# Optimization experiments

Measured on AMD Instinct MI355X. Metric: run time of the kernel, lower is better.

## Reference

```python
import jax, jax.numpy as jnp
import numpy as np

B, C, P, NG, NCLS, HID, N, IMG = 2, 256, 7, 2, 81, 1024, 512, 800
STRIDES = [4, 8, 16, 32]
SCALE = 56.0  # roi_map_level_scale


def _roi_align(feat, rois, pooled, scale, ng):
    """torchvision-legacy (aligned=False) ROI Align. feat [B,C,H,W], rois [N,5]."""
    Bf, Cf, H, W = feat.shape
    ft = jnp.transpose(feat, (0, 2, 3, 1))  # [B,H,W,C]
    b = rois[:, 0].astype(jnp.int32)
    x1, y1, x2, y2 = (rois[:, i] * scale for i in (1, 2, 3, 4))
    rw = jnp.maximum(x2 - x1, 1.0)
    rh = jnp.maximum(y2 - y1, 1.0)
    # sample grid per output bin: ng points per axis, centered in sub-bins
    g = (jnp.arange(pooled)[:, None] + (jnp.arange(ng)[None, :] + 0.5) / ng).reshape(-1)  # [P*ng]
    ys = y1[:, None] + g[None, :] * (rh / pooled)[:, None]  # [N,S]
    xs = x1[:, None] + g[None, :] * (rw / pooled)[:, None]

    def axis(coord, size):
        valid = (coord >= -1.0) & (coord <= size)
        c = jnp.clip(coord, 0.0, size - 1)
        lo = jnp.floor(c).astype(jnp.int32)
        hi = jnp.minimum(lo + 1, size - 1)
        return valid, lo, hi, c - lo

    vy, ylo, yhi, fy = axis(ys, H)
    vx, xlo, xhi, fx = axis(xs, W)
    bb = b[:, None, None]

    def gather(yi, xi):
        return ft[bb, yi[:, :, None], xi[:, None, :], :]  # [N,S,S,C]

    wy = fy[:, :, None, None]
    wx = fx[:, None, :, None]
    val = ((1 - wy) * (1 - wx) * gather(ylo, xlo) + (1 - wy) * wx * gather(ylo, xhi)
           + wy * (1 - wx) * gather(yhi, xlo) + wy * wx * gather(yhi, xhi))
    val = jnp.where((vy[:, :, None] & vx[:, None, :])[..., None], val, 0.0)
    val = val.reshape(-1, pooled, ng, pooled, ng, Cf).mean(axis=(2, 4))  # [N,P,P,C]
    return jnp.transpose(val, (0, 3, 1, 2))  # [N,C,P,P]


def setup_inputs() -> dict:
    key = jax.random.key(0)
    ks = jax.random.split(key, 16)
    feats = {}
    for i, s in enumerate(STRIDES):
        hw = IMG // s
        feats[f"p{i+2}"] = jax.random.normal(ks[i], (B, C, hw, hw), jnp.float32)
    # realistic proposals: batch idx + boxes with sizes 16..512 px
    bidx = jax.random.randint(ks[4], (N,), 0, B).astype(jnp.float32)
    sw = 2.0 ** jax.random.uniform(ks[5], (N,), minval=4.0, maxval=9.0)
    sh = 2.0 ** jax.random.uniform(ks[6], (N,), minval=4.0, maxval=9.0)
    x1 = jax.random.uniform(ks[7], (N,)) * (IMG - sw)
    y1 = jax.random.uniform(ks[8], (N,)) * (IMG - sh)
    rois = jnp.stack([bidx, x1, y1, x1 + sw - 1, y1 + sh - 1], axis=1)
    D = C * P * P
    inp = dict(feats, rois=rois,
               w1=0.01 * jax.random.normal(ks[9], (HID, D), jnp.float32),
               b1=jnp.zeros((HID,), jnp.float32),
               w2=0.01 * jax.random.normal(ks[10], (HID, HID), jnp.float32),
               b2=jnp.zeros((HID,), jnp.float32),
               w_cls=0.01 * jax.random.normal(ks[11], (NCLS, HID), jnp.float32),
               b_cls=jnp.zeros((NCLS,), jnp.float32),
               w_reg=0.001 * jax.random.normal(ks[12], (NCLS * 4, HID), jnp.float32),
               b_reg=jnp.zeros((NCLS * 4,), jnp.float32))
    return inp


def reference(p2, p3, p4, p5, rois, w1, b1, w2, b2, w_cls, b_cls, w_reg, b_reg):
    feats = [p2, p3, p4, p5]
    # FPN level assignment (same math as torch: log2(sqrt(hw)/scale + 1e-6), floor, clamp)
    rh = rois[:, 4] - rois[:, 2] + 1
    rw = rois[:, 3] - rois[:, 1] + 1
    levels = jnp.clip(jnp.floor(jnp.log2(jnp.sqrt(rh * rw) / SCALE + 1e-6)), 0, 3).astype(jnp.int32)
    # dispatch: compute each ROI on its assigned level (masked combine == gather/sort-scatter)
    pooled = jnp.zeros((rois.shape[0], C, P, P), rois.dtype)
    for l, feat in enumerate(feats):
        pl = _roi_align(feat, rois, P, 1.0 / STRIDES[l], NG)
        pooled = pooled + jnp.where((levels == l)[:, None, None, None], pl, 0.0)
    x = pooled.reshape(pooled.shape[0], -1)  # [N, C*P*P]
    x = jax.nn.relu(x @ w1.T + b1)
    x = jax.nn.relu(x @ w2.T + b2)
    x_cls = x @ w_cls.T + b_cls
    x_reg = x @ w_reg.T + b_reg  # TEST mode, not class-agnostic: no gather
    cls_probs = jax.nn.softmax(x_cls, axis=1)
    rois_out = rois.reshape(B, -1, 5)
    cls_probs = cls_probs.reshape(B, rois_out.shape[1], -1)
    bbox_preds = x_reg.reshape(B, rois_out.shape[1], -1)
    return rois_out, cls_probs, bbox_preds
```

## Files before the change

kernel.cpp:

```cpp
#include <hip/hip_runtime.h>
#include <hip/hip_bf16.h>
#include <math.h>

#define NROI   512
#define CCH    256
#define POOLP  7
#define DDIM   12544
#define HIDN   1024
#define NCLS   81
#define NREG   324
#define NHEAD  512
#define OUT_ROIS   2560
#define OUT_CLS    (512*81)

typedef __attribute__((ext_vector_type(4))) float f32x4;
typedef __attribute__((ext_vector_type(8))) short bf16x8;

static __device__ __forceinline__ unsigned short f2bf(float x) {
    __hip_bfloat16 h = __float2bfloat16(x);
    return *reinterpret_cast<unsigned short*>(&h);
}
static __device__ __forceinline__ float bf2f(unsigned short u) {
    unsigned int b = ((unsigned int)u) << 16;
    return *reinterpret_cast<float*>(&b);
}

__global__ void copy_rois_k(const float* __restrict__ rois, float* __restrict__ out) {
    int i = blockIdx.x * 256 + threadIdx.x;
    if (i < OUT_ROIS) out[i] = rois[i];
}

__global__ __launch_bounds__(256) void cvt_bf16_k(const float4* __restrict__ in,
                                                  ushort4* __restrict__ out, int n4) {
    int i = blockIdx.x * 256 + threadIdx.x;
    if (i >= n4) return;
    float4 v = in[i];
    ushort4 o;
    o.x = f2bf(v.x); o.y = f2bf(v.y); o.z = f2bf(v.z); o.w = f2bf(v.w);
    out[i] = o;
}

__global__ __launch_bounds__(256) void pack_head_k(const float* __restrict__ wc,
                                                   const float* __restrict__ wr,
                                                   unsigned short* __restrict__ Wh) {
    int i = blockIdx.x * 256 + threadIdx.x;
    int r = i >> 10, c = i & 1023;
    float v = (r < NCLS) ? wc[r * HIDN + c]
            : (r < NCLS + NREG) ? wr[(r - NCLS) * HIDN + c] : 0.f;
    Wh[i] = f2bf(v);
}

__global__ __launch_bounds__(256) void permute_w1_k(const float* __restrict__ w1,
                                                    unsigned short* __restrict__ w1b) {
    __shared__ unsigned short lw[49 * 258];
    int n = blockIdx.x, t = threadIdx.x;
    const float* src = w1 + (size_t)n * DDIM;
#pragma unroll
    for (int k = t; k < DDIM; k += 256) {
        int c = k / 49;
        int s = k - c * 49;
        lw[s * 258 + c] = f2bf(src[k]);
    }
    __syncthreads();
    unsigned int* dst = (unsigned int*)(w1b + (size_t)n * DDIM);
    for (int j2 = t; j2 < DDIM / 2; j2 += 256) {
        int s  = j2 >> 7;
        int c2 = (j2 & 127) << 1;
        unsigned int v = lw[s * 258 + c2] | ((unsigned int)lw[s * 258 + c2 + 1] << 16);
        dst[j2] = v;
    }
}

__global__ __launch_bounds__(256) void transpose_cvt_k(const float* __restrict__ in,
                                                       unsigned short* __restrict__ out,
                                                       int S) {
    __shared__ float tile[32][33];
    int b  = blockIdx.z;
    int s0 = blockIdx.x * 32, c0 = blockIdx.y * 32;
    int s  = s0 + threadIdx.x;
#pragma unroll
    for (int j = 0; j < 32; j += 8) {
        int c = c0 + threadIdx.y + j;
        tile[threadIdx.y + j][threadIdx.x] = (s < S) ? in[((size_t)b * CCH + c) * S + s] : 0.f;
    }
    __syncthreads();
    int c = c0 + threadIdx.x;
#pragma unroll
    for (int j = 0; j < 32; j += 8) {
        int s2 = s0 + threadIdx.y + j;
        if (s2 < S) out[((size_t)b * S + s2) * CCH + c] = f2bf(tile[threadIdx.x][threadIdx.y + j]);
    }
}

__global__ __launch_bounds__(256) void roi_align_k(const unsigned short* __restrict__ f0,
                                                   const unsigned short* __restrict__ f1,
                                                   const unsigned short* __restrict__ f2,
                                                   const unsigned short* __restrict__ f3,
                                                   const float* __restrict__ rois,
                                                   unsigned short* __restrict__ xpool) {
    __shared__ float s_f[16];
    __shared__ int   s_lo[16], s_hi[16], s_v[16];

    int py = blockIdx.x, r = blockIdx.y, t = threadIdx.x;

    float r0  = rois[r * 5 + 0];
    float rx1 = rois[r * 5 + 1], ry1 = rois[r * 5 + 2];
    float rx2 = rois[r * 5 + 3], ry2 = rois[r * 5 + 4];
    int b = (int)r0;

    float aw = rx2 - rx1 + 1.f, ah = ry2 - ry1 + 1.f;
    float lvf = floorf(log2f(sqrtf(ah * aw) / 56.f + 1e-6f));
    int lv = (int)fminf(fmaxf(lvf, 0.f), 3.f);

    const unsigned short* F = (lv == 0) ? f0 : (lv == 1) ? f1 : (lv == 2) ? f2 : f3;
    int HW      = (lv == 0) ? 200 : (lv == 1) ? 100 : (lv == 2) ? 50 : 25;
    float scale = (lv == 0) ? 0.25f : (lv == 1) ? 0.125f : (lv == 2) ? 0.0625f : 0.03125f;

    float x1 = rx1 * scale, yy1 = ry1 * scale;
    float x2 = rx2 * scale, yy2 = ry2 * scale;
    float rw = fmaxf(x2 - x1, 1.f), rh = fmaxf(yy2 - yy1, 1.f);

    if (t < 16) {
        bool isY = t < 2;
        float coord;
        if (isY) {
            float g = (float)py + ((float)t + 0.5f) * 0.5f;
            coord = yy1 + g * (rh * (1.f / 7.f));
        } else {
            int j = t - 2;
            float g = (float)(j >> 1) + ((float)(j & 1) + 0.5f) * 0.5f;
            coord = x1 + g * (rw * (1.f / 7.f));
        }
        int vld = (coord >= -1.f && coord <= (float)HW) ? 1 : 0;
        float c = fminf(fmaxf(coord, 0.f), (float)(HW - 1));
        int lo  = (int)floorf(c);
        int hi  = min(lo + 1, HW - 1);
        s_v[t] = vld; s_lo[t] = lo; s_hi[t] = hi; s_f[t] = c - (float)lo;
    }
    __syncthreads();

    const unsigned short* Fb = F + ((size_t)b * HW * HW) * CCH + t;
    size_t obase = (size_t)r * DDIM + py * 7 * 256 + t;

    for (int px = 0; px < POOLP; px++) {
        float acc = 0.f;
#pragma unroll
        for (int s = 0; s < 4; s++) {
            int iy = s >> 1;
            int ix = px * 2 + (s & 1);
            int vy = s_v[iy], vx = s_v[2 + ix];
            if (vy & vx) {
                float fy = s_f[iy], fx = s_f[2 + ix];
                int ylo = s_lo[iy], yhi = s_hi[iy];
                int xlo = s_lo[2 + ix], xhi = s_hi[2 + ix];
                float v00 = bf2f(Fb[((size_t)ylo * HW + xlo) * CCH]);
                float v01 = bf2f(Fb[((size_t)ylo * HW + xhi) * CCH]);
                float v10 = bf2f(Fb[((size_t)yhi * HW + xlo) * CCH]);
                float v11 = bf2f(Fb[((size_t)yhi * HW + xhi) * CCH]);
                acc += (1.f - fy) * ((1.f - fx) * v00 + fx * v01)
                     + fy * ((1.f - fx) * v10 + fx * v11);
            }
        }
        xpool[obase + px * 256] = f2bf(acc * 0.25f);
    }
}

__global__ __launch_bounds__(256) void roi_align_nchw_k(const float* __restrict__ f0,
                                                        const float* __restrict__ f1,
                                                        const float* __restrict__ f2,
                                                        const float* __restrict__ f3,
                                                        const float* __restrict__ rois,
                                                        unsigned short* __restrict__ xpool) {
    __shared__ float s_f[16];
    __shared__ int   s_lo[16], s_hi[16], s_v[16];
    int py = blockIdx.x, r = blockIdx.y, t = threadIdx.x;
    float r0  = rois[r * 5 + 0];
    float rx1 = rois[r * 5 + 1], ry1 = rois[r * 5 + 2];
    float rx2 = rois[r * 5 + 3], ry2 = rois[r * 5 + 4];
    int b = (int)r0;
    float aw = rx2 - rx1 + 1.f, ah = ry2 - ry1 + 1.f;
    float lvf = floorf(log2f(sqrtf(ah * aw) / 56.f + 1e-6f));
    int lv = (int)fminf(fmaxf(lvf, 0.f), 3.f);
    const float* F = (lv == 0) ? f0 : (lv == 1) ? f1 : (lv == 2) ? f2 : f3;
    int HW      = (lv == 0) ? 200 : (lv == 1) ? 100 : (lv == 2) ? 50 : 25;
    float scale = (lv == 0) ? 0.25f : (lv == 1) ? 0.125f : (lv == 2) ? 0.0625f : 0.03125f;
    float x1 = rx1 * scale, yy1 = ry1 * scale;
    float x2 = rx2 * scale, yy2 = ry2 * scale;
    float rw = fmaxf(x2 - x1, 1.f), rh = fmaxf(yy2 - yy1, 1.f);
    if (t < 16) {
        bool isY = t < 2;
        float coord;
        if (isY) {
            float g = (float)py + ((float)t + 0.5f) * 0.5f;
            coord = yy1 + g * (rh * (1.f / 7.f));
        } else {
            int j = t - 2;
            float g = (float)(j >> 1) + ((float)(j & 1) + 0.5f) * 0.5f;
            coord = x1 + g * (rw * (1.f / 7.f));
        }
        int vld = (coord >= -1.f && coord <= (float)HW) ? 1 : 0;
        float c = fminf(fmaxf(coord, 0.f), (float)(HW - 1));
        int lo  = (int)floorf(c);
        int hi  = min(lo + 1, HW - 1);
        s_v[t] = vld; s_lo[t] = lo; s_hi[t] = hi; s_f[t] = c - (float)lo;
    }
    __syncthreads();
    const float* Fb = F + ((size_t)b * CCH + t) * HW * HW;
    size_t obase = (size_t)r * DDIM + py * 7 * 256 + t;
    for (int px = 0; px < POOLP; px++) {
        float acc = 0.f;
#pragma unroll
        for (int s = 0; s < 4; s++) {
            int iy = s >> 1, ix = px * 2 + (s & 1);
            int vy = s_v[iy], vx = s_v[2 + ix];
            if (vy & vx) {
                float fy = s_f[iy], fx = s_f[2 + ix];
                int ylo = s_lo[iy], yhi = s_hi[iy];
                int xlo = s_lo[2 + ix], xhi = s_hi[2 + ix];
                float v00 = Fb[(size_t)ylo * HW + xlo];
                float v01 = Fb[(size_t)ylo * HW + xhi];
                float v10 = Fb[(size_t)yhi * HW + xlo];
                float v11 = Fb[(size_t)yhi * HW + xhi];
                acc += (1.f - fy) * ((1.f - fx) * v00 + fx * v01)
                     + fy * ((1.f - fx) * v10 + fx * v11);
            }
        }
        xpool[obase + px * 256] = f2bf(acc * 0.25f);
    }
}

__global__ __launch_bounds__(256) void gemm_bf16_k(const unsigned short* __restrict__ A,
                                                   const unsigned short* __restrict__ W,
                                                   float* __restrict__ Cp,
                                                   int M, int N, int K, int kchunk) {
    __shared__ __align__(16) unsigned short As[8][64][8];
    __shared__ __align__(16) unsigned short Ws[8][64][8];

    int t = threadIdx.x;
    int lane = t & 63, wid = t >> 6;
    int m0 = blockIdx.y * 64, n0 = blockIdx.x * 64;
    int k0 = blockIdx.z * kchunk;
    int wm = (wid >> 1) * 32, wn = (wid & 1) * 32;
    int fr = lane & 15, kg = lane >> 4;

    f32x4 acc[2][2] = {};

    const unsigned short* Arow = A + (size_t)(m0 + lane) * K;
    const unsigned short* Wrow = W + (size_t)(n0 + lane) * K;

    for (int kb = k0; kb < k0 + kchunk; kb += 64) {
#pragma unroll
        for (int i = 0; i < 2; i++) {
            int c = wid * 2 + i;
            __builtin_amdgcn_global_load_lds(
                (const __attribute__((address_space(1))) void*)(Arow + kb + c * 8),
                (__attribute__((address_space(3))) void*)(&As[c][0][0]), 16, 0, 0);
            __builtin_amdgcn_global_load_lds(
                (const __attribute__((address_space(1))) void*)(Wrow + kb + c * 8),
                (__attribute__((address_space(3))) void*)(&Ws[c][0][0]), 16, 0, 0);
        }
        __syncthreads();
#pragma unroll
        for (int h = 0; h < 2; h++) {
            bf16x8 a0 = *(const bf16x8*)(&As[h * 4 + kg][wm + fr][0]);
            bf16x8 a1 = *(const bf16x8*)(&As[h * 4 + kg][wm + 16 + fr][0]);
            bf16x8 b0 = *(const bf16x8*)(&Ws[h * 4 + kg][wn + fr][0]);
            bf16x8 b1 = *(const bf16x8*)(&Ws[h * 4 + kg][wn + 16 + fr][0]);
            acc[0][0] = __builtin_amdgcn_mfma_f32_16x16x32_bf16(a0, b0, acc[0][0], 0, 0, 0);
            acc[0][1] = __builtin_amdgcn_mfma_f32_16x16x32_bf16(a0, b1, acc[0][1], 0, 0, 0);
            acc[1][0] = __builtin_amdgcn_mfma_f32_16x16x32_bf16(a1, b0, acc[1][0], 0, 0, 0);
            acc[1][1] = __builtin_amdgcn_mfma_f32_16x16x32_bf16(a1, b1, acc[1][1], 0, 0, 0);
        }
        __syncthreads();
    }

    float* Cout = Cp + (size_t)blockIdx.z * M * N;
    int row = m0 + wm + (lane >> 4) * 4;
    int col = n0 + wn + (lane & 15);
#pragma unroll
    for (int fm = 0; fm < 2; fm++)
#pragma unroll
        for (int fn = 0; fn < 2; fn++)
#pragma unroll
            for (int r = 0; r < 4; r++)
                Cout[(size_t)(row + fm * 16 + r) * N + col + fn * 16] = acc[fm][fn][r];
}

__global__ __launch_bounds__(256) void gemm128_bf16_k(const unsigned short* __restrict__ A,
                                                      const unsigned short* __restrict__ W,
                                                      float* __restrict__ Cp,
                                                      int M, int N, int K, int kchunk) {
    __shared__ __align__(16) unsigned short As[8][128][8];
    __shared__ __align__(16) unsigned short Ws[8][128][8];

    int t = threadIdx.x;
    int lane = t & 63, wid = t >> 6;
    int m0 = blockIdx.y * 128, n0 = blockIdx.x * 128;
    int k0 = blockIdx.z * kchunk;
    int wm = (wid >> 1) * 64, wn = (wid & 1) * 64;
    int fr = lane & 15, kg = lane >> 4;

    f32x4 acc[4][4] = {};

    for (int kb = k0; kb < k0 + kchunk; kb += 64) {
#pragma unroll
        for (int i = 0; i < 4; i++) {
            int c   = wid * 4 + i;
            int kgc = c >> 1;
            int r0w = (c & 1) * 64;
            __builtin_amdgcn_global_load_lds(
                (const __attribute__((address_space(1))) void*)
                    (A + (size_t)(m0 + r0w + lane) * K + kb + kgc * 8),
                (__attribute__((address_space(3))) void*)(&As[kgc][r0w][0]), 16, 0, 0);
            __builtin_amdgcn_global_load_lds(
                (const __attribute__((address_space(1))) void*)
                    (W + (size_t)(n0 + r0w + lane) * K + kb + kgc * 8),
                (__attribute__((address_space(3))) void*)(&Ws[kgc][r0w][0]), 16, 0, 0);
        }
        __syncthreads();
#pragma unroll
        for (int h = 0; h < 2; h++) {
            bf16x8 av[4], bv[4];
#pragma unroll
            for (int f = 0; f < 4; f++) {
                av[f] = *(const bf16x8*)(&As[h * 4 + kg][wm + f * 16 + fr][0]);
                bv[f] = *(const bf16x8*)(&Ws[h * 4 + kg][wn + f * 16 + fr][0]);
            }
#pragma unroll
            for (int fm = 0; fm < 4; fm++)
#pragma unroll
                for (int fn = 0; fn < 4; fn++)
                    acc[fm][fn] = __builtin_amdgcn_mfma_f32_16x16x32_bf16(
                        av[fm], bv[fn], acc[fm][fn], 0, 0, 0);
        }
        __syncthreads();
    }

    float* Cout = Cp + (size_t)blockIdx.z * M * N;
    int row = m0 + wm + (lane >> 4) * 4;
    int col = n0 + wn + (lane & 15);
#pragma unroll
    for (int fm = 0; fm < 4; fm++)
#pragma unroll
        for (int fn = 0; fn < 4; fn++)
#pragma unroll
            for (int r = 0; r < 4; r++)
                Cout[(size_t)(row + fm * 16 + r) * N + col + fn * 16] = acc[fm][fn][r];
}

__global__ __launch_bounds__(256) void reduce_relu_k(const float* __restrict__ Cp,
                                                     const float* __restrict__ bias,
                                                     unsigned short* __restrict__ out,
                                                     int MN, int ks) {
    int i = blockIdx.x * 256 + threadIdx.x;
    if (i >= MN) return;
    float s = 0.f;
    for (int p = 0; p < ks; p++) s += Cp[(size_t)p * MN + i];
    s = fmaxf(s + bias[i & (HIDN - 1)], 0.f);
    out[i] = f2bf(s);
}

__global__ __launch_bounds__(256) void head_reduce_k(const float* __restrict__ Cp,
                                                     const float* __restrict__ bc,
                                                     const float* __restrict__ br,
                                                     float* __restrict__ cls_logits,
                                                     float* __restrict__ reg_out, int ks) {
    int i = blockIdx.x * 256 + threadIdx.x;
    int r = i >> 9, c = i & 511;
    float s = 0.f;
    for (int p = 0; p < ks; p++) s += Cp[(size_t)p * (512 * 512) + i];
    if (c < NCLS) cls_logits[r * NCLS + c] = s + bc[c];
    else if (c < NCLS + NREG) reg_out[r * NREG + (c - NCLS)] = s + br[c - NCLS];
}

__global__ void softmax81_k(const float* __restrict__ logits, float* __restrict__ out) {
    int r = blockIdx.x;
    int l = threadIdx.x;
    float v0 = logits[r * NCLS + l];
    float v1 = (l + 64 < NCLS) ? logits[r * NCLS + l + 64] : -INFINITY;
    float m = fmaxf(v0, v1);
#pragma unroll
    for (int o = 32; o; o >>= 1) m = fmaxf(m, __shfl_xor(m, o));
    float e0 = __expf(v0 - m);
    float e1 = (l + 64 < NCLS) ? __expf(v1 - m) : 0.f;
    float s = e0 + e1;
#pragma unroll
    for (int o = 32; o; o >>= 1) s += __shfl_xor(s, o);
    float inv = 1.f / s;
    out[r * NCLS + l] = e0 * inv;
    if (l + 64 < NCLS) out[r * NCLS + l + 64] = e1 * inv;
}

extern "C" void kernel_launch(void* const* d_in, const int* in_sizes, int n_in,
                              void* d_out, int out_size, void* d_ws, size_t ws_size,
                              hipStream_t stream) {
    const float* p2   = (const float*)d_in[0];
    const float* p3   = (const float*)d_in[1];
    const float* p4   = (const float*)d_in[2];
    const float* p5   = (const float*)d_in[3];
    const float* rois = (const float*)d_in[4];
    const float* w1   = (const float*)d_in[5];
    const float* b1   = (const float*)d_in[6];
    const float* w2   = (const float*)d_in[7];
    const float* b2   = (const float*)d_in[8];
    const float* wc   = (const float*)d_in[9];
    const float* bc   = (const float*)d_in[10];
    const float* wr   = (const float*)d_in[11];
    const float* br   = (const float*)d_in[12];

    float* out = (float*)d_out;

    const int KS1 = 14;

    char* p = (char*)d_ws;
    auto alloc = [&](size_t bytes) { char* r = p; p += (bytes + 255) & ~(size_t)255; return r; };
    unsigned short* xpool = (unsigned short*)alloc((size_t)NROI * DDIM * 2);
    unsigned short* y1b   = (unsigned short*)alloc((size_t)NROI * HIDN * 2);
    unsigned short* y2b   = (unsigned short*)alloc((size_t)NROI * HIDN * 2);
    unsigned short* w1b   = (unsigned short*)alloc((size_t)HIDN * DDIM * 2);
    unsigned short* w2b   = (unsigned short*)alloc((size_t)HIDN * HIDN * 2);
    unsigned short* whd   = (unsigned short*)alloc((size_t)NHEAD * HIDN * 2);
    float*          clsl  = (float*)alloc((size_t)NROI * NCLS * 4);
    float*          part  = (float*)alloc((size_t)KS1 * NROI * HIDN * 4);
    unsigned short* ft0 = (unsigned short*)alloc((size_t)2 * 40000 * CCH * 2);
    unsigned short* ft1 = (unsigned short*)alloc((size_t)2 * 10000 * CCH * 2);
    unsigned short* ft2 = (unsigned short*)alloc((size_t)2 * 2500 * CCH * 2);
    unsigned short* ft3 = (unsigned short*)alloc((size_t)2 * 625 * CCH * 2);
    bool nhwc = (size_t)(p - (char*)d_ws) <= ws_size;

    copy_rois_k<<<(OUT_ROIS + 255) / 256, 256, 0, stream>>>(rois, out);

    permute_w1_k<<<HIDN, 256, 0, stream>>>(w1, w1b);
    cvt_bf16_k<<<(HIDN * HIDN / 4 + 255) / 256, 256, 0, stream>>>(
        (const float4*)w2, (ushort4*)w2b, HIDN * HIDN / 4);
    pack_head_k<<<(NHEAD * HIDN + 255) / 256, 256, 0, stream>>>(wc, wr, whd);

    if (nhwc) {
        dim3 blk(32, 8);
        transpose_cvt_k<<<dim3(1250, 8, 2), blk, 0, stream>>>(p2, ft0, 40000);
        transpose_cvt_k<<<dim3(313, 8, 2),  blk, 0, stream>>>(p3, ft1, 10000);
        transpose_cvt_k<<<dim3(79, 8, 2),   blk, 0, stream>>>(p4, ft2, 2500);
        transpose_cvt_k<<<dim3(20, 8, 2),   blk, 0, stream>>>(p5, ft3, 625);
        roi_align_k<<<dim3(POOLP, NROI), 256, 0, stream>>>(ft0, ft1, ft2, ft3, rois, xpool);
    } else {
        roi_align_nchw_k<<<dim3(POOLP, NROI), 256, 0, stream>>>(p2, p3, p4, p5, rois, xpool);
    }

    gemm128_bf16_k<<<dim3(HIDN / 128, NROI / 128, KS1), 256, 0, stream>>>(
        xpool, w1b, part, NROI, HIDN, DDIM, DDIM / KS1);
    reduce_relu_k<<<(NROI * HIDN + 255) / 256, 256, 0, stream>>>(
        part, b1, y1b, NROI * HIDN, KS1);

    gemm_bf16_k<<<dim3(HIDN / 64, NROI / 64, 2), 256, 0, stream>>>(
        y1b, w2b, part, NROI, HIDN, HIDN, HIDN / 2);
    reduce_relu_k<<<(NROI * HIDN + 255) / 256, 256, 0, stream>>>(
        part, b2, y2b, NROI * HIDN, 2);

    gemm_bf16_k<<<dim3(NHEAD / 64, NROI / 64, 4), 256, 0, stream>>>(
        y2b, whd, part, NROI, NHEAD, HIDN, HIDN / 4);
    head_reduce_k<<<(NROI * NHEAD + 255) / 256, 256, 0, stream>>>(
        part, bc, br, clsl, out + OUT_ROIS + OUT_CLS, 4);

    softmax81_k<<<NROI, 64, 0, stream>>>(clsl, out + OUT_ROIS);
}
```

Before: 172.4 us.

## Fuse prep and transpose kernels, use atomic split-K accumulation, swizzle GEMM blocks

Several small prep kernels (roi copy, w2 convert, head pack) are merged into one launch that also zeroes the accumulators. The four per-level NHWC transposes become one launch that packs bf16 pairs on store. The split-K GEMMs now atomically add into a single fp32 buffer instead of writing partials, which replaces the multi-partial reduce with a light bias/relu epilogue. The head bias and softmax are fused into one kernel, and the first GEMM uses a remapped block order for better L2 locality. Atomics add contention, and the summation order becomes nondeterministic.

```diff
diff --git a/kernel.cpp b/kernel.cpp
--- a/kernel.cpp
+++ b/kernel.cpp
@@ -25,29 +25,40 @@
     return *reinterpret_cast<float*>(&b);
 }
 
-__global__ void copy_rois_k(const float* __restrict__ rois, float* __restrict__ out) {
-    int i = blockIdx.x * 256 + threadIdx.x;
-    if (i < OUT_ROIS) out[i] = rois[i];
-}
-
-__global__ __launch_bounds__(256) void cvt_bf16_k(const float4* __restrict__ in,
-                                                  ushort4* __restrict__ out, int n4) {
-    int i = blockIdx.x * 256 + threadIdx.x;
-    if (i >= n4) return;
-    float4 v = in[i];
-    ushort4 o;
-    o.x = f2bf(v.x); o.y = f2bf(v.y); o.z = f2bf(v.z); o.w = f2bf(v.w);
-    out[i] = o;
-}
-
-__global__ __launch_bounds__(256) void pack_head_k(const float* __restrict__ wc,
-                                                   const float* __restrict__ wr,
-                                                   unsigned short* __restrict__ Wh) {
-    int i = blockIdx.x * 256 + threadIdx.x;
-    int r = i >> 10, c = i & 1023;
-    float v = (r < NCLS) ? wc[r * HIDN + c]
-            : (r < NCLS + NREG) ? wr[(r - NCLS) * HIDN + c] : 0.f;
-    Wh[i] = f2bf(v);
+#define PREP_B0 10
+#define PREP_B1 (PREP_B0 + 1280)
+#define PREP_B2 (PREP_B1 + 1024)
+#define PREP_B3 (PREP_B2 + 1024)
+__global__ __launch_bounds__(256) void prep_k(const float* __restrict__ rois,
+                                              const float* __restrict__ w2,
+                                              const float* __restrict__ wc,
+                                              const float* __restrict__ wr,
+                                              float* __restrict__ out,
+                                              float* __restrict__ accz,
+                                              unsigned short* __restrict__ w2b,
+                                              unsigned short* __restrict__ whd) {
+    int bid = blockIdx.x, t = threadIdx.x;
+    if (bid < PREP_B0) {
+        int i = bid * 256 + t;
+        if (i < OUT_ROIS) out[i] = rois[i];
+    } else if (bid < PREP_B1) {
+        int i = (bid - PREP_B0) * 256 + t;
+        ((float4*)accz)[i] = make_float4(0.f, 0.f, 0.f, 0.f);
+    } else if (bid < PREP_B2) {
+        int i = (bid - PREP_B1) * 256 + t;
+        float4 v = ((const float4*)w2)[i];
+        ushort4 o;
+        o.x = f2bf(v.x); o.y = f2bf(v.y); o.z = f2bf(v.z); o.w = f2bf(v.w);
+        ((ushort4*)w2b)[i] = o;
+    } else {
+        int i2 = (bid - PREP_B2) * 256 + t;
+        int r = i2 >> 9, c = (i2 & 511) << 1;
+        float v0, v1;
+        if (r < NCLS)             { v0 = wc[r * HIDN + c]; v1 = wc[r * HIDN + c + 1]; }
+        else if (r < NCLS + NREG) { v0 = wr[(r - NCLS) * HIDN + c]; v1 = wr[(r - NCLS) * HIDN + c + 1]; }
+        else                      { v0 = 0.f; v1 = 0.f; }
+        ((unsigned int*)whd)[i2] = (unsigned int)f2bf(v0) | ((unsigned int)f2bf(v1) << 16);
+    }
 }
 
 __global__ __launch_bounds__(256) void permute_w1_k(const float* __restrict__ w1,
@@ -66,29 +77,49 @@
     for (int j2 = t; j2 < DDIM / 2; j2 += 256) {
         int s  = j2 >> 7;
         int c2 = (j2 & 127) << 1;
-        unsigned int v = lw[s * 258 + c2] | ((unsigned int)lw[s * 258 + c2 + 1] << 16);
-        dst[j2] = v;
-    }
-}
-
-__global__ __launch_bounds__(256) void transpose_cvt_k(const float* __restrict__ in,
-                                                       unsigned short* __restrict__ out,
-                                                       int S) {
-    __shared__ float tile[32][33];
+        dst[j2] = lw[s * 258 + c2] | ((unsigned int)lw[s * 258 + c2 + 1] << 16);
+    }
+}
+
+__global__ __launch_bounds__(256) void transpose_all_k(const float* __restrict__ p2,
+                                                       const float* __restrict__ p3,
+                                                       const float* __restrict__ p4,
+                                                       const float* __restrict__ p5,
+                                                       unsigned short* __restrict__ f0,
+                                                       unsigned short* __restrict__ f1,
+                                                       unsigned short* __restrict__ f2,
+                                                       unsigned short* __restrict__ f3) {
+    __shared__ unsigned short tile[32][66];
+    int xb = blockIdx.x;
+    const float* in; unsigned short* outp; int S, base;
+    if (xb < 1250)      { in = p2; outp = f0; S = 40000; base = 0; }
+    else if (xb < 1563) { in = p3; outp = f1; S = 10000; base = 1250; }
+    else if (xb < 1642) { in = p4; outp = f2; S = 2500;  base = 1563; }
+    else                { in = p5; outp = f3; S = 625;   base = 1642; }
+    int s0 = (xb - base) * 32;
+    int c0 = blockIdx.y * 64;
     int b  = blockIdx.z;
-    int s0 = blockIdx.x * 32, c0 = blockIdx.y * 32;
-    int s  = s0 + threadIdx.x;
-#pragma unroll
-    for (int j = 0; j < 32; j += 8) {
-        int c = c0 + threadIdx.y + j;
-        tile[threadIdx.y + j][threadIdx.x] = (s < S) ? in[((size_t)b * CCH + c) * S + s] : 0.f;
+    int t  = threadIdx.x;
+
+    {
+        int sL = t & 31, cq = t >> 5;
+        const float* src = in + ((size_t)b * CCH + c0 + cq * 8) * S + s0 + sL;
+        bool ok = (s0 + sL) < S;
+#pragma unroll
+        for (int j = 0; j < 8; j++)
+            tile[sL][cq * 8 + j] = ok ? f2bf(src[(size_t)j * S]) : (unsigned short)0;
     }
     __syncthreads();
-    int c = c0 + threadIdx.x;
-#pragma unroll
-    for (int j = 0; j < 32; j += 8) {
-        int s2 = s0 + threadIdx.y + j;
-        if (s2 < S) out[((size_t)b * S + s2) * CCH + c] = f2bf(tile[threadIdx.x][threadIdx.y + j]);
+    {
+        int c2 = t & 31, sq = t >> 5;
+#pragma unroll
+        for (int i = 0; i < 4; i++) {
+            int s = sq * 4 + i;
+            if (s0 + s < S) {
+                unsigned int v = tile[s][c2 * 2] | ((unsigned int)tile[s][c2 * 2 + 1] << 16);
+                ((unsigned int*)(outp + ((size_t)b * S + s0 + s) * CCH + c0))[c2] = v;
+            }
+        }
     }
 }
 
@@ -231,7 +262,7 @@
 
 __global__ __launch_bounds__(256) void gemm_bf16_k(const unsigned short* __restrict__ A,
                                                    const unsigned short* __restrict__ W,
-                                                   float* __restrict__ Cp,
+                                                   float* __restrict__ Cacc,
                                                    int M, int N, int K, int kchunk) {
     __shared__ __align__(16) unsigned short As[8][64][8];
     __shared__ __align__(16) unsigned short Ws[8][64][8];
@@ -274,7 +305,6 @@
         __syncthreads();
     }
 
-    float* Cout = Cp + (size_t)blockIdx.z * M * N;
     int row = m0 + wm + (lane >> 4) * 4;
     int col = n0 + wn + (lane & 15);
 #pragma unroll
@@ -283,20 +313,25 @@
         for (int fn = 0; fn < 2; fn++)
 #pragma unroll
             for (int r = 0; r < 4; r++)
-                Cout[(size_t)(row + fm * 16 + r) * N + col + fn * 16] = acc[fm][fn][r];
+                atomicAdd(&Cacc[(size_t)(row + fm * 16 + r) * N + col + fn * 16],
+                          acc[fm][fn][r]);
 }
 
 __global__ __launch_bounds__(256) void gemm128_bf16_k(const unsigned short* __restrict__ A,
                                                       const unsigned short* __restrict__ W,
-                                                      float* __restrict__ Cp,
+                                                      float* __restrict__ Cacc,
                                                       int M, int N, int K, int kchunk) {
     __shared__ __align__(16) unsigned short As[8][128][8];
     __shared__ __align__(16) unsigned short Ws[8][128][8];
 
+    int lin = blockIdx.x;
+    int nb  = (lin & 7) * 56 + (lin >> 3);
+    int bx = nb & 7, by = (nb >> 3) & 3, bz = nb >> 5;
+
     int t = threadIdx.x;
     int lane = t & 63, wid = t >> 6;
-    int m0 = blockIdx.y * 128, n0 = blockIdx.x * 128;
-    int k0 = blockIdx.z * kchunk;
+    int m0 = by * 128, n0 = bx * 128;
+    int k0 = bz * kchunk;
     int wm = (wid >> 1) * 64, wn = (wid & 1) * 64;
     int fr = lane & 15, kg = lane >> 4;
 
@@ -336,7 +371,6 @@
         __syncthreads();
     }
 
-    float* Cout = Cp + (size_t)blockIdx.z * M * N;
     int row = m0 + wm + (lane >> 4) * 4;
     int col = n0 + wn + (lane & 15);
 #pragma unroll
@@ -345,39 +379,31 @@
         for (int fn = 0; fn < 4; fn++)
 #pragma unroll
             for (int r = 0; r < 4; r++)
-                Cout[(size_t)(row + fm * 16 + r) * N + col + fn * 16] = acc[fm][fn][r];
-}
-
-__global__ __launch_bounds__(256) void reduce_relu_k(const float* __restrict__ Cp,
-                                                     const float* __restrict__ bias,
-                                                     unsigned short* __restrict__ out,
-                                                     int MN, int ks) {
+                atomicAdd(&Cacc[(size_t)(row + fm * 16 + r) * N + col + fn * 16],
+                          acc[fm][fn][r]);
+}
+
+__global__ __launch_bounds__(256) void fc_ep_k(const float* __restrict__ acc,
+                                               const float* __restrict__ bias,
+                                               unsigned short* __restrict__ dst, int MN) {
     int i = blockIdx.x * 256 + threadIdx.x;
     if (i >= MN) return;
-    float s = 0.f;
-    for (int p = 0; p < ks; p++) s += Cp[(size_t)p * MN + i];
-    s = fmaxf(s + bias[i & (HIDN - 1)], 0.f);
-    out[i] = f2bf(s);
-}
-
-__global__ __launch_bounds__(256) void head_reduce_k(const float* __restrict__ Cp,
-                                                     const float* __restrict__ bc,
-                                                     const float* __restrict__ br,
-                                                     float* __restrict__ cls_logits,
-                                                     float* __restrict__ reg_out, int ks) {
-    int i = blockIdx.x * 256 + threadIdx.x;
-    int r = i >> 9, c = i & 511;
-    float s = 0.f;
-    for (int p = 0; p < ks; p++) s += Cp[(size_t)p * (512 * 512) + i];
-    if (c < NCLS) cls_logits[r * NCLS + c] = s + bc[c];
-    else if (c < NCLS + NREG) reg_out[r * NREG + (c - NCLS)] = s + br[c - NCLS];
-}
-
-__global__ void softmax81_k(const float* __restrict__ logits, float* __restrict__ out) {
-    int r = blockIdx.x;
-    int l = threadIdx.x;
-    float v0 = logits[r * NCLS + l];
-    float v1 = (l + 64 < NCLS) ? logits[r * NCLS + l + 64] : -INFINITY;
+    float s = fmaxf(acc[i] + bias[i & (HIDN - 1)], 0.f);
+    dst[i] = f2bf(s);
+}
+
+__global__ void head_ep_k(const float* __restrict__ hf,
+                          const float* __restrict__ bc,
+                          const float* __restrict__ br,
+                          float* __restrict__ out) {
+    int r = blockIdx.x, l = threadIdx.x;
+    const float* row = hf + (size_t)r * NHEAD;
+
+    float* reg = out + OUT_ROIS + OUT_CLS + (size_t)r * NREG;
+    for (int j = l; j < NREG; j += 64) reg[j] = row[NCLS + j] + br[j];
+
+    float v0 = row[l] + bc[l];
+    float v1 = (l + 64 < NCLS) ? row[l + 64] + bc[l + 64] : -INFINITY;
     float m = fmaxf(v0, v1);
 #pragma unroll
     for (int o = 32; o; o >>= 1) m = fmaxf(m, __shfl_xor(m, o));
@@ -387,8 +413,9 @@
 #pragma unroll
     for (int o = 32; o; o >>= 1) s += __shfl_xor(s, o);
     float inv = 1.f / s;
-    out[r * NCLS + l] = e0 * inv;
-    if (l + 64 < NCLS) out[r * NCLS + l + 64] = e1 * inv;
+    float* cls = out + OUT_ROIS + (size_t)r * NCLS;
+    cls[l] = e0 * inv;
+    if (l + 64 < NCLS) cls[l + 64] = e1 * inv;
 }
 
 extern "C" void kernel_launch(void* const* d_in, const int* in_sizes, int n_in,
@@ -420,46 +447,37 @@
     unsigned short* w1b   = (unsigned short*)alloc((size_t)HIDN * DDIM * 2);
     unsigned short* w2b   = (unsigned short*)alloc((size_t)HIDN * HIDN * 2);
     unsigned short* whd   = (unsigned short*)alloc((size_t)NHEAD * HIDN * 2);
-    float*          clsl  = (float*)alloc((size_t)NROI * NCLS * 4);
-    float*          part  = (float*)alloc((size_t)KS1 * NROI * HIDN * 4);
+    float*          accz  = (float*)alloc((size_t)(NROI * HIDN * 2 + NROI * NHEAD) * 4);
     unsigned short* ft0 = (unsigned short*)alloc((size_t)2 * 40000 * CCH * 2);
     unsigned short* ft1 = (unsigned short*)alloc((size_t)2 * 10000 * CCH * 2);
     unsigned short* ft2 = (unsigned short*)alloc((size_t)2 * 2500 * CCH * 2);
     unsigned short* ft3 = (unsigned short*)alloc((size_t)2 * 625 * CCH * 2);
     bool nhwc = (size_t)(p - (char*)d_ws) <= ws_size;
 
-    copy_rois_k<<<(OUT_ROIS + 255) / 256, 256, 0, stream>>>(rois, out);
-
+    float* y1f = accz;
+    float* y2f = accz + (size_t)NROI * HIDN;
+    float* hf  = accz + (size_t)NROI * HIDN * 2;
+
+    prep_k<<<PREP_B3, 256, 0, stream>>>(rois, w2, wc, wr, out, accz, w2b, whd);
     permute_w1_k<<<HIDN, 256, 0, stream>>>(w1, w1b);
-    cvt_bf16_k<<<(HIDN * HIDN / 4 + 255) / 256, 256, 0, stream>>>(
-        (const float4*)w2, (ushort4*)w2b, HIDN * HIDN / 4);
-    pack_head_k<<<(NHEAD * HIDN + 255) / 256, 256, 0, stream>>>(wc, wr, whd);
 
     if (nhwc) {
-        dim3 blk(32, 8);
-        transpose_cvt_k<<<dim3(1250, 8, 2), blk, 0, stream>>>(p2, ft0, 40000);
-        transpose_cvt_k<<<dim3(313, 8, 2),  blk, 0, stream>>>(p3, ft1, 10000);
-        transpose_cvt_k<<<dim3(79, 8, 2),   blk, 0, stream>>>(p4, ft2, 2500);
-        transpose_cvt_k<<<dim3(20, 8, 2),   blk, 0, stream>>>(p5, ft3, 625);
+        transpose_all_k<<<dim3(1662, 4, 2), 256, 0, stream>>>(p2, p3, p4, p5,
+                                                              ft0, ft1, ft2, ft3);
         roi_align_k<<<dim3(POOLP, NROI), 256, 0, stream>>>(ft0, ft1, ft2, ft3, rois, xpool);
     } else {
         roi_align_nchw_k<<<dim3(POOLP, NROI), 256, 0, stream>>>(p2, p3, p4, p5, rois, xpool);
     }
 
-    gemm128_bf16_k<<<dim3(HIDN / 128, NROI / 128, KS1), 256, 0, stream>>>(
-        xpool, w1b, part, NROI, HIDN, DDIM, DDIM / KS1);
-    reduce_relu_k<<<(NROI * HIDN + 255) / 256, 256, 0, stream>>>(
-        part, b1, y1b, NROI * HIDN, KS1);
+    gemm128_bf16_k<<<8 * 4 * KS1, 256, 0, stream>>>(
+        xpool, w1b, y1f, NROI, HIDN, DDIM, DDIM / KS1);
+    fc_ep_k<<<(NROI * HIDN + 255) / 256, 256, 0, stream>>>(y1f, b1, y1b, NROI * HIDN);
 
     gemm_bf16_k<<<dim3(HIDN / 64, NROI / 64, 2), 256, 0, stream>>>(
-        y1b, w2b, part, NROI, HIDN, HIDN, HIDN / 2);
-    reduce_relu_k<<<(NROI * HIDN + 255) / 256, 256, 0, stream>>>(
-        part, b2, y2b, NROI * HIDN, 2);
+        y1b, w2b, y2f, NROI, HIDN, HIDN, HIDN / 2);
+    fc_ep_k<<<(NROI * HIDN + 255) / 256, 256, 0, stream>>>(y2f, b2, y2b, NROI * HIDN);
 
     gemm_bf16_k<<<dim3(NHEAD / 64, NROI / 64, 4), 256, 0, stream>>>(
-        y2b, whd, part, NROI, NHEAD, HIDN, HIDN / 4);
-    head_reduce_k<<<(NROI * NHEAD + 255) / 256, 256, 0, stream>>>(
-        part, bc, br, clsl, out + OUT_ROIS + OUT_CLS, 4);
-
-    softmax81_k<<<NROI, 64, 0, stream>>>(clsl, out + OUT_ROIS);
-}
+        y2b, whd, hf, NROI, NHEAD, HIDN, HIDN / 4);
+    head_ep_k<<<NROI, 64, 0, stream>>>(hf, bc, br, out);
+}
```

New measurement: 163.2 us. 1.06x faster.
